# Performance work log

Hardware: AMD Instinct MI355X
Metric: run time of the kernel (lower is better)

Reference implementation:

```python
import jax, jax.numpy as jnp
import numpy as np

B, N, E, D, H = 8, 5000, 160000, 64, 128  # batch, nodes, edges, gnn hidden, head hidden


def _w(key, shape, scale=0.05):
    return jax.random.normal(key, shape, jnp.float32) * scale


def setup_inputs() -> dict:
    key = jax.random.key(0)
    ks = jax.random.split(key, 24)
    inp = {
        "x": jax.random.normal(ks[0], (B, N), jnp.float32),
        "edges": jax.random.randint(ks[1], (E, 2), 0, N, dtype=jnp.int32),
        "emb": _w(ks[2], (N, D)),
        # conv1: prepare FFN (2 layers, no bias, elu), update FFN (2 layers, bias)
        "c1_pw1": _w(ks[3], (D, D)), "c1_pw2": _w(ks[4], (D, D)),
        "c1_uw1": _w(ks[5], (2 * D, D)), "c1_ub1": jnp.zeros((D,), jnp.float32),
        "c1_uw2": _w(ks[6], (D, D)), "c1_ub2": jnp.zeros((D,), jnp.float32),
        # conv2
        "c2_pw1": _w(ks[7], (D, D)), "c2_pw2": _w(ks[8], (D, D)),
        "c2_uw1": _w(ks[9], (2 * D, D)), "c2_ub1": jnp.zeros((D,), jnp.float32),
        "c2_uw2": _w(ks[10], (D, D)), "c2_ub2": jnp.zeros((D,), jnp.float32),
        # TARnet prob heads: flatten -> Dense(H, elu) -> Dense(2) (mu, log_sigma)
        "w0a": _w(ks[11], (N * D, H), 0.005), "b0a": jnp.zeros((H,), jnp.float32),
        "w0b": _w(ks[12], (H, 2)), "b0b": jnp.zeros((2,), jnp.float32),
        "w1a": _w(ks[13], (N * D, H), 0.005), "b1a": jnp.zeros((H,), jnp.float32),
        "w1b": _w(ks[14], (H, 2)), "b1b": jnp.zeros((2,), jnp.float32),
    }
    return inp


def _graph_conv(h, edges, pw1, pw2, uw1, ub1, uw2, ub2):
    # h: [B, N, D]; edges: [E, 2] (parent, node)
    parents = jnp.take(h, edges[:, 0], axis=1)            # [B, E, D] gather
    m = jax.nn.elu(parents @ pw1)                          # prepare FFN (no bias)
    m = jax.nn.elu(m @ pw2)
    agg = jnp.zeros_like(h).at[:, edges[:, 1]].add(m)      # unsorted_segment_sum -> [B, N, D]
    hcat = jnp.concatenate([h, agg], axis=-1)              # combination_type='concat'
    u = jax.nn.elu(hcat @ uw1 + ub1)                       # update FFN
    return u @ uw2 + ub2                                   # final_activation=None


def reference(x, edges, emb,
              c1_pw1, c1_pw2, c1_uw1, c1_ub1, c1_uw2, c1_ub2,
              c2_pw1, c2_pw2, c2_uw1, c2_ub1, c2_uw2, c2_ub2,
              w0a, b0a, w0b, b0b, w1a, b1a, w1b, b1b):
    # node features scale learned per-node embeddings -> [B, N, D]
    h = x[:, :, None] * emb[None, :, :]
    h = _graph_conv(h, edges, c1_pw1, c1_pw2, c1_uw1, c1_ub1, c1_uw2, c1_ub2)
    h = _graph_conv(h, edges, c2_pw1, c2_pw2, c2_uw1, c2_ub1, c2_uw2, c2_ub2)
    phi = h.reshape(h.shape[0], -1)                        # flatten [B, N*D]
    y0 = jax.nn.elu(phi @ w0a + b0a) @ w0b + b0b           # [B, 2] (mu, log_sigma)
    y1 = jax.nn.elu(phi @ w1a + b1a) @ w1b + b1b           # [B, 2]
    return jnp.concatenate([y0, y1], axis=1)               # [B, 4]
```

## Files before the change

kernel.cpp:

```cpp
#include <hip/hip_runtime.h>


constexpr int B = 8, N = 5000, E = 160000, D = 64, H = 128;
constexpr int BN = B * N;
constexpr int ND = N * D;
constexpr long BND = (long)BN * D;

__device__ __forceinline__ float elu_f(float x) {
    return x > 0.0f ? x : __expf(x) - 1.0f;
}

__global__ __launch_bounds__(256) void k_scale(const float* __restrict__ x,
                                               const float* __restrict__ emb,
                                               float* __restrict__ h) {
    int idx = blockIdx.x * 256 + threadIdx.x;
    int d4 = idx & 15;
    int bn = idx >> 4;
    int n  = bn % N;
    float xs = x[bn];
    float4 e = reinterpret_cast<const float4*>(emb)[n * (D / 4) + d4];
    reinterpret_cast<float4*>(h)[idx] = make_float4(xs * e.x, xs * e.y, xs * e.z, xs * e.w);
}

__global__ __launch_bounds__(256) void k_count(const int* __restrict__ edges,
                                               int* __restrict__ cnt) {
    int i = blockIdx.x * 256 + threadIdx.x;
    if (i < E) atomicAdd(&cnt[edges[2 * i + 1]], 1);
}

__global__ __launch_bounds__(256) void k_scan(const int* __restrict__ cnt,
                                              int* __restrict__ offs) {
    __shared__ int part[256];
    int t = threadIdx.x;
    const int CH = 20;
    int base = t * CH;
    int s = 0;
    for (int i = 0; i < CH; ++i) { int idx = base + i; if (idx < N) s += cnt[idx]; }
    part[t] = s;
    __syncthreads();
    for (int off = 1; off < 256; off <<= 1) {
        int add = (t >= off) ? part[t - off] : 0;
        __syncthreads();
        part[t] += add;
        __syncthreads();
    }
    int run = part[t] - s;
    for (int i = 0; i < CH; ++i) {
        int idx = base + i;
        if (idx < N) { offs[idx] = run; run += cnt[idx]; }
    }
    if (t == 255) offs[N] = run;
}

__global__ __launch_bounds__(256) void k_fill(const int* __restrict__ edges,
                                              const int* __restrict__ offs,
                                              int* __restrict__ cursor,
                                              int* __restrict__ elist) {
    int i = blockIdx.x * 256 + threadIdx.x;
    if (i < E) {
        int child = edges[2 * i + 1];
        int pos = offs[child] + atomicAdd(&cursor[child], 1);
        elist[pos] = edges[2 * i];
    }
}

__global__ __launch_bounds__(256) void k_prepare(const float* __restrict__ hin,
                                                 const float* __restrict__ W1,
                                                 const float* __restrict__ W2,
                                                 float* __restrict__ M) {
    __shared__ float sW1[64 * 64];
    __shared__ float sW2[64 * 64];
    __shared__ float sP[64 * 65];
    int t = threadIdx.x;
    long r0 = (long)blockIdx.x * 64;
    for (int i = t; i < 4096; i += 256) { sW1[i] = W1[i]; sW2[i] = W2[i]; }
    int lane = t & 63, rq = t >> 6;
    for (int r = rq; r < 64; r += 4)
        sP[r * 65 + lane] = hin[(r0 + r) * 64 + lane];
    __syncthreads();

    int cg = t & 15, rg = t >> 4;
    float acc[4][4] = {};
    #pragma unroll 8
    for (int k = 0; k < 64; ++k) {
        float a[4];
        #pragma unroll
        for (int i = 0; i < 4; ++i) a[i] = sP[(rg * 4 + i) * 65 + k];
        float4 bb = *reinterpret_cast<const float4*>(&sW1[k * 64 + cg * 4]);
        #pragma unroll
        for (int i = 0; i < 4; ++i) {
            acc[i][0] += a[i] * bb.x; acc[i][1] += a[i] * bb.y;
            acc[i][2] += a[i] * bb.z; acc[i][3] += a[i] * bb.w;
        }
    }
    __syncthreads();
    #pragma unroll
    for (int i = 0; i < 4; ++i)
        #pragma unroll
        for (int j = 0; j < 4; ++j)
            sP[(rg * 4 + i) * 65 + cg * 4 + j] = elu_f(acc[i][j]);
    __syncthreads();

    float acc2[4][4] = {};
    #pragma unroll 8
    for (int k = 0; k < 64; ++k) {
        float a[4];
        #pragma unroll
        for (int i = 0; i < 4; ++i) a[i] = sP[(rg * 4 + i) * 65 + k];
        float4 bb = *reinterpret_cast<const float4*>(&sW2[k * 64 + cg * 4]);
        #pragma unroll
        for (int i = 0; i < 4; ++i) {
            acc2[i][0] += a[i] * bb.x; acc2[i][1] += a[i] * bb.y;
            acc2[i][2] += a[i] * bb.z; acc2[i][3] += a[i] * bb.w;
        }
    }
    #pragma unroll
    for (int i = 0; i < 4; ++i) {
        float4 o = make_float4(elu_f(acc2[i][0]), elu_f(acc2[i][1]),
                               elu_f(acc2[i][2]), elu_f(acc2[i][3]));
        *reinterpret_cast<float4*>(&M[(r0 + rg * 4 + i) * 64 + cg * 4]) = o;
    }
}

__global__ __launch_bounds__(256) void k_aggregate(const float* __restrict__ M,
                                                   const int* __restrict__ offs,
                                                   const int* __restrict__ elist,
                                                   float* __restrict__ agg) {
    int t = threadIdx.x;
    int lane = t & 63, unit = t >> 6;
    long bn = (long)blockIdx.x * 4 + unit;
    int b = (int)(bn / N);
    int n = (int)(bn - (long)b * N);
    int e0 = offs[n], e1 = offs[n + 1];
    const float* Mb = M + (long)b * N * 64;
    float acc = 0.0f;
    for (int e = e0; e < e1; ++e) {
        int p = elist[e];
        acc += Mb[(long)p * 64 + lane];
    }
    agg[bn * 64 + lane] = acc;
}

__global__ __launch_bounds__(256) void k_update1(const float* __restrict__ h,
                                                 const float* __restrict__ agg,
                                                 const float* __restrict__ W,
                                                 const float* __restrict__ bias,
                                                 float* __restrict__ u) {
    __shared__ float sW[128 * 64];
    __shared__ float sP[32 * 129];
    int t = threadIdx.x;
    long r0 = (long)blockIdx.x * 32;
    for (int i = t; i < 128 * 64; i += 256) sW[i] = W[i];
    for (int i = t; i < 32 * 128; i += 256) {
        int r = i >> 7, k = i & 127;
        long row = r0 + r;
        float v = (k < 64) ? h[row * 64 + k] : agg[row * 64 + (k - 64)];
        sP[r * 129 + k] = v;
    }
    __syncthreads();
    int cg = t & 15, rg = t >> 4;
    float acc[2][4] = {};
    #pragma unroll 8
    for (int k = 0; k < 128; ++k) {
        float a0 = sP[(rg * 2 + 0) * 129 + k];
        float a1 = sP[(rg * 2 + 1) * 129 + k];
        float4 bb = *reinterpret_cast<const float4*>(&sW[k * 64 + cg * 4]);
        acc[0][0] += a0 * bb.x; acc[0][1] += a0 * bb.y; acc[0][2] += a0 * bb.z; acc[0][3] += a0 * bb.w;
        acc[1][0] += a1 * bb.x; acc[1][1] += a1 * bb.y; acc[1][2] += a1 * bb.z; acc[1][3] += a1 * bb.w;
    }
    float4 b4 = *reinterpret_cast<const float4*>(&bias[cg * 4]);
    #pragma unroll
    for (int i = 0; i < 2; ++i) {
        float4 o = make_float4(elu_f(acc[i][0] + b4.x), elu_f(acc[i][1] + b4.y),
                               elu_f(acc[i][2] + b4.z), elu_f(acc[i][3] + b4.w));
        *reinterpret_cast<float4*>(&u[(r0 + rg * 2 + i) * 64 + cg * 4]) = o;
    }
}

__global__ __launch_bounds__(256) void k_update2(const float* __restrict__ u,
                                                 const float* __restrict__ W,
                                                 const float* __restrict__ bias,
                                                 float* __restrict__ hout) {
    __shared__ float sW[64 * 64];
    __shared__ float sP[32 * 65];
    int t = threadIdx.x;
    long r0 = (long)blockIdx.x * 32;
    for (int i = t; i < 4096; i += 256) sW[i] = W[i];
    for (int i = t; i < 32 * 64; i += 256) {
        int r = i >> 6, k = i & 63;
        sP[r * 65 + k] = u[(r0 + r) * 64 + k];
    }
    __syncthreads();
    int cg = t & 15, rg = t >> 4;
    float acc[2][4] = {};
    #pragma unroll 8
    for (int k = 0; k < 64; ++k) {
        float a0 = sP[(rg * 2 + 0) * 65 + k];
        float a1 = sP[(rg * 2 + 1) * 65 + k];
        float4 bb = *reinterpret_cast<const float4*>(&sW[k * 64 + cg * 4]);
        acc[0][0] += a0 * bb.x; acc[0][1] += a0 * bb.y; acc[0][2] += a0 * bb.z; acc[0][3] += a0 * bb.w;
        acc[1][0] += a1 * bb.x; acc[1][1] += a1 * bb.y; acc[1][2] += a1 * bb.z; acc[1][3] += a1 * bb.w;
    }
    float4 b4 = *reinterpret_cast<const float4*>(&bias[cg * 4]);
    #pragma unroll
    for (int i = 0; i < 2; ++i) {
        float4 o = make_float4(acc[i][0] + b4.x, acc[i][1] + b4.y,
                               acc[i][2] + b4.z, acc[i][3] + b4.w);
        *reinterpret_cast<float4*>(&hout[(r0 + rg * 2 + i) * 64 + cg * 4]) = o;
    }
}

__global__ __launch_bounds__(128) void k_head(const float* __restrict__ phi,
                                              const float* __restrict__ w0a,
                                              const float* __restrict__ w1a,
                                              float* __restrict__ hidden) {
    const float* wa = blockIdx.y ? w1a : w0a;
    float* hid = hidden + blockIdx.y * (8 * H);
    int h = threadIdx.x;
    int k0 = blockIdx.x * 320;
    float acc[8] = {};
    #pragma unroll 8
    for (int kk = 0; kk < 320; ++kk) {
        int k = k0 + kk;
        float w = wa[(long)k * H + h];
        #pragma unroll
        for (int b2 = 0; b2 < 8; ++b2)
            acc[b2] += phi[b2 * ND + k] * w;
    }
    #pragma unroll
    for (int b2 = 0; b2 < 8; ++b2)
        unsafeAtomicAdd(&hid[b2 * H + h], acc[b2]);
}

__global__ __launch_bounds__(64) void k_final(const float* __restrict__ hidden,
                                              const float* __restrict__ b0a,
                                              const float* __restrict__ w0b,
                                              const float* __restrict__ b0b,
                                              const float* __restrict__ b1a,
                                              const float* __restrict__ w1b,
                                              const float* __restrict__ b1b,
                                              float* __restrict__ out) {
    int t = threadIdx.x;
    if (t >= 32) return;
    int head = t >> 4, b = (t >> 1) & 7, j = t & 1;
    const float* hid = hidden + head * (8 * H) + b * H;
    const float* ba = head ? b1a : b0a;
    const float* wb = head ? w1b : w0b;
    const float* bb = head ? b1b : b0b;
    float acc = 0.0f;
    for (int hh = 0; hh < H; ++hh)
        acc += elu_f(hid[hh] + ba[hh]) * wb[hh * 2 + j];
    out[b * 4 + head * 2 + j] = acc + bb[j];
}

extern "C" void kernel_launch(void* const* d_in, const int* in_sizes, int n_in,
                              void* d_out, int out_size, void* d_ws, size_t ws_size,
                              hipStream_t stream) {
    const float* x      = (const float*)d_in[0];
    const int*   edges  = (const int*)d_in[1];
    const float* emb    = (const float*)d_in[2];
    const float* c1_pw1 = (const float*)d_in[3];
    const float* c1_pw2 = (const float*)d_in[4];
    const float* c1_uw1 = (const float*)d_in[5];
    const float* c1_ub1 = (const float*)d_in[6];
    const float* c1_uw2 = (const float*)d_in[7];
    const float* c1_ub2 = (const float*)d_in[8];
    const float* c2_pw1 = (const float*)d_in[9];
    const float* c2_pw2 = (const float*)d_in[10];
    const float* c2_uw1 = (const float*)d_in[11];
    const float* c2_ub1 = (const float*)d_in[12];
    const float* c2_uw2 = (const float*)d_in[13];
    const float* c2_ub2 = (const float*)d_in[14];
    const float* w0a    = (const float*)d_in[15];
    const float* b0a    = (const float*)d_in[16];
    const float* w0b    = (const float*)d_in[17];
    const float* b0b    = (const float*)d_in[18];
    const float* w1a    = (const float*)d_in[19];
    const float* b1a    = (const float*)d_in[20];
    const float* w1b    = (const float*)d_in[21];
    const float* b1b    = (const float*)d_in[22];
    float* out = (float*)d_out;

    float* hA     = (float*)d_ws;
    float* hB     = hA + BND;
    float* Mu     = hB + BND;
    float* agg    = Mu + BND;
    float* hidden = agg + BND;
    int* cnt      = (int*)(hidden + 2048);
    int* offs     = cnt + N;
    int* cursor   = offs + N + 1;
    int* elist    = cursor + N;

    hipMemsetAsync(cnt, 0, N * sizeof(int), stream);
    hipMemsetAsync(cursor, 0, N * sizeof(int), stream);
    hipMemsetAsync(hidden, 0, 2 * 8 * H * sizeof(float), stream);

    k_scale<<<2500, 256, 0, stream>>>(x, emb, hA);

    k_count<<<E / 256, 256, 0, stream>>>(edges, cnt);
    k_scan<<<1, 256, 0, stream>>>(cnt, offs);
    k_fill<<<E / 256, 256, 0, stream>>>(edges, offs, cursor, elist);

    k_prepare<<<BN / 64, 256, 0, stream>>>(hA, c1_pw1, c1_pw2, Mu);
    k_aggregate<<<BN / 4, 256, 0, stream>>>(Mu, offs, elist, agg);
    k_update1<<<BN / 32, 256, 0, stream>>>(hA, agg, c1_uw1, c1_ub1, Mu);
    k_update2<<<BN / 32, 256, 0, stream>>>(Mu, c1_uw2, c1_ub2, hB);

    k_prepare<<<BN / 64, 256, 0, stream>>>(hB, c2_pw1, c2_pw2, Mu);
    k_aggregate<<<BN / 4, 256, 0, stream>>>(Mu, offs, elist, agg);
    k_update1<<<BN / 32, 256, 0, stream>>>(hB, agg, c2_uw1, c2_ub1, Mu);
    k_update2<<<BN / 32, 256, 0, stream>>>(Mu, c2_uw2, c2_ub2, hA);

    k_head<<<dim3(ND / 320, 2), 128, 0, stream>>>(hA, w0a, w1a, hidden);
    k_final<<<1, 64, 0, stream>>>(hidden, b0a, w0b, b0b, b1a, w1b, b1b, out);
}
```

Before: 730.4 us.

## Fuse scale into prepare, merge update kernels, vectorize aggregate and head GEMV

```diff
diff --git a/kernel.cpp b/kernel.cpp
--- a/kernel.cpp
+++ b/kernel.cpp
@@ -5,21 +5,10 @@
 constexpr int BN = B * N;
 constexpr int ND = N * D;
 constexpr long BND = (long)BN * D;
+constexpr int KC = 640;
 
 __device__ __forceinline__ float elu_f(float x) {
     return x > 0.0f ? x : __expf(x) - 1.0f;
-}
-
-__global__ __launch_bounds__(256) void k_scale(const float* __restrict__ x,
-                                               const float* __restrict__ emb,
-                                               float* __restrict__ h) {
-    int idx = blockIdx.x * 256 + threadIdx.x;
-    int d4 = idx & 15;
-    int bn = idx >> 4;
-    int n  = bn % N;
-    float xs = x[bn];
-    float4 e = reinterpret_cast<const float4*>(emb)[n * (D / 4) + d4];
-    reinterpret_cast<float4*>(h)[idx] = make_float4(xs * e.x, xs * e.y, xs * e.z, xs * e.w);
 }
 
 __global__ __launch_bounds__(256) void k_count(const int* __restrict__ edges,
@@ -64,24 +53,42 @@
     }
 }
 
-__global__ __launch_bounds__(256) void k_prepare(const float* __restrict__ hin,
+__global__ __launch_bounds__(512) void k_prepare(const float* __restrict__ xsrc,
+                                                 const float* __restrict__ emb,
+                                                 const float* __restrict__ hin,
                                                  const float* __restrict__ W1,
                                                  const float* __restrict__ W2,
-                                                 float* __restrict__ M) {
+                                                 float* __restrict__ M,
+                                                 float* __restrict__ hwt) {
     __shared__ float sW1[64 * 64];
-    __shared__ float sW2[64 * 64];
-    __shared__ float sP[64 * 65];
-    int t = threadIdx.x;
-    long r0 = (long)blockIdx.x * 64;
-    for (int i = t; i < 4096; i += 256) { sW1[i] = W1[i]; sW2[i] = W2[i]; }
-    int lane = t & 63, rq = t >> 6;
-    for (int r = rq; r < 64; r += 4)
-        sP[r * 65 + lane] = hin[(r0 + r) * 64 + lane];
+    __shared__ float sP[128 * 65];
+    int t = threadIdx.x;
+    int r0 = blockIdx.x * 128;
+    for (int i = t; i < 4096; i += 512) sW1[i] = W1[i];
+    if (xsrc) {
+        for (int i = t; i < 128 * 64; i += 512) {
+            int r = i >> 6, c = i & 63;
+            int row = r0 + r;
+            float v = 0.0f;
+            if (row < BN) {
+                int n = row % N;
+                v = xsrc[row] * emb[n * 64 + c];
+                hwt[(long)row * 64 + c] = v;
+            }
+            sP[r * 65 + c] = v;
+        }
+    } else {
+        for (int i = t; i < 128 * 64; i += 512) {
+            int r = i >> 6, c = i & 63;
+            int row = r0 + r;
+            sP[r * 65 + c] = (row < BN) ? hin[(long)row * 64 + c] : 0.0f;
+        }
+    }
     __syncthreads();
 
     int cg = t & 15, rg = t >> 4;
     float acc[4][4] = {};
-    #pragma unroll 8
+    #pragma unroll 4
     for (int k = 0; k < 64; ++k) {
         float a[4];
         #pragma unroll
@@ -102,12 +109,12 @@
     __syncthreads();
 
     float acc2[4][4] = {};
-    #pragma unroll 8
+    #pragma unroll 4
     for (int k = 0; k < 64; ++k) {
         float a[4];
         #pragma unroll
         for (int i = 0; i < 4; ++i) a[i] = sP[(rg * 4 + i) * 65 + k];
-        float4 bb = *reinterpret_cast<const float4*>(&sW2[k * 64 + cg * 4]);
+        float4 bb = *reinterpret_cast<const float4*>(&W2[k * 64 + cg * 4]);
         #pragma unroll
         for (int i = 0; i < 4; ++i) {
             acc2[i][0] += a[i] * bb.x; acc2[i][1] += a[i] * bb.y;
@@ -116,9 +123,12 @@
     }
     #pragma unroll
     for (int i = 0; i < 4; ++i) {
-        float4 o = make_float4(elu_f(acc2[i][0]), elu_f(acc2[i][1]),
-                               elu_f(acc2[i][2]), elu_f(acc2[i][3]));
-        *reinterpret_cast<float4*>(&M[(r0 + rg * 4 + i) * 64 + cg * 4]) = o;
+        int row = r0 + rg * 4 + i;
+        if (row < BN) {
+            float4 o = make_float4(elu_f(acc2[i][0]), elu_f(acc2[i][1]),
+                                   elu_f(acc2[i][2]), elu_f(acc2[i][3]));
+            *reinterpret_cast<float4*>(&M[(long)row * 64 + cg * 4]) = o;
+        }
     }
 }
 
@@ -127,109 +137,146 @@
                                                    const int* __restrict__ elist,
                                                    float* __restrict__ agg) {
     int t = threadIdx.x;
-    int lane = t & 63, unit = t >> 6;
-    long bn = (long)blockIdx.x * 4 + unit;
-    int b = (int)(bn / N);
-    int n = (int)(bn - (long)b * N);
+    int lane = t & 63, wv = t >> 6;
+    int bn = blockIdx.x * 4 + wv;
+    int b = bn / N;
+    int n = bn - b * N;
     int e0 = offs[n], e1 = offs[n + 1];
-    const float* Mb = M + (long)b * N * 64;
-    float acc = 0.0f;
-    for (int e = e0; e < e1; ++e) {
+    const float* Mb = M + (long)b * ND;
+    int h4 = lane & 15, le = lane >> 4;
+    float4 acc = make_float4(0.f, 0.f, 0.f, 0.f);
+    for (int e = e0 + le; e < e1; e += 4) {
         int p = elist[e];
-        acc += Mb[(long)p * 64 + lane];
-    }
-    agg[bn * 64 + lane] = acc;
-}
-
-__global__ __launch_bounds__(256) void k_update1(const float* __restrict__ h,
-                                                 const float* __restrict__ agg,
-                                                 const float* __restrict__ W,
-                                                 const float* __restrict__ bias,
-                                                 float* __restrict__ u) {
-    __shared__ float sW[128 * 64];
-    __shared__ float sP[32 * 129];
-    int t = threadIdx.x;
-    long r0 = (long)blockIdx.x * 32;
-    for (int i = t; i < 128 * 64; i += 256) sW[i] = W[i];
-    for (int i = t; i < 32 * 128; i += 256) {
+        float4 v = *reinterpret_cast<const float4*>(&Mb[(long)p * 64 + h4 * 4]);
+        acc.x += v.x; acc.y += v.y; acc.z += v.z; acc.w += v.w;
+    }
+    #pragma unroll
+    for (int m = 16; m <= 32; m <<= 1) {
+        acc.x += __shfl_xor(acc.x, m);
+        acc.y += __shfl_xor(acc.y, m);
+        acc.z += __shfl_xor(acc.z, m);
+        acc.w += __shfl_xor(acc.w, m);
+    }
+    if (le == 0)
+        *reinterpret_cast<float4*>(&agg[(long)bn * 64 + h4 * 4]) = acc;
+}
+
+__global__ __launch_bounds__(512) void k_update(const float* __restrict__ h,
+                                                const float* __restrict__ agg,
+                                                const float* __restrict__ W1,
+                                                const float* __restrict__ b1,
+                                                const float* __restrict__ W2,
+                                                const float* __restrict__ b2,
+                                                float* __restrict__ hout) {
+    __shared__ float sW1[128 * 64];
+    __shared__ float sP[64 * 129];
+    int t = threadIdx.x;
+    long r0 = (long)blockIdx.x * 64;
+    for (int i = t; i < 128 * 64; i += 512) sW1[i] = W1[i];
+    for (int i = t; i < 64 * 128; i += 512) {
         int r = i >> 7, k = i & 127;
         long row = r0 + r;
         float v = (k < 64) ? h[row * 64 + k] : agg[row * 64 + (k - 64)];
         sP[r * 129 + k] = v;
     }
     __syncthreads();
+
     int cg = t & 15, rg = t >> 4;
     float acc[2][4] = {};
-    #pragma unroll 8
+    #pragma unroll 4
     for (int k = 0; k < 128; ++k) {
         float a0 = sP[(rg * 2 + 0) * 129 + k];
         float a1 = sP[(rg * 2 + 1) * 129 + k];
-        float4 bb = *reinterpret_cast<const float4*>(&sW[k * 64 + cg * 4]);
+        float4 bb = *reinterpret_cast<const float4*>(&sW1[k * 64 + cg * 4]);
         acc[0][0] += a0 * bb.x; acc[0][1] += a0 * bb.y; acc[0][2] += a0 * bb.z; acc[0][3] += a0 * bb.w;
         acc[1][0] += a1 * bb.x; acc[1][1] += a1 * bb.y; acc[1][2] += a1 * bb.z; acc[1][3] += a1 * bb.w;
     }
-    float4 b4 = *reinterpret_cast<const float4*>(&bias[cg * 4]);
+    float4 bv1 = *reinterpret_cast<const float4*>(&b1[cg * 4]);
+    __syncthreads();
     #pragma unroll
     for (int i = 0; i < 2; ++i) {
-        float4 o = make_float4(elu_f(acc[i][0] + b4.x), elu_f(acc[i][1] + b4.y),
-                               elu_f(acc[i][2] + b4.z), elu_f(acc[i][3] + b4.w));
-        *reinterpret_cast<float4*>(&u[(r0 + rg * 2 + i) * 64 + cg * 4]) = o;
-    }
-}
-
-__global__ __launch_bounds__(256) void k_update2(const float* __restrict__ u,
-                                                 const float* __restrict__ W,
-                                                 const float* __restrict__ bias,
-                                                 float* __restrict__ hout) {
-    __shared__ float sW[64 * 64];
-    __shared__ float sP[32 * 65];
-    int t = threadIdx.x;
-    long r0 = (long)blockIdx.x * 32;
-    for (int i = t; i < 4096; i += 256) sW[i] = W[i];
-    for (int i = t; i < 32 * 64; i += 256) {
-        int r = i >> 6, k = i & 63;
-        sP[r * 65 + k] = u[(r0 + r) * 64 + k];
-    }
-    __syncthreads();
-    int cg = t & 15, rg = t >> 4;
-    float acc[2][4] = {};
-    #pragma unroll 8
+        sP[(rg * 2 + i) * 129 + cg * 4 + 0] = elu_f(acc[i][0] + bv1.x);
+        sP[(rg * 2 + i) * 129 + cg * 4 + 1] = elu_f(acc[i][1] + bv1.y);
+        sP[(rg * 2 + i) * 129 + cg * 4 + 2] = elu_f(acc[i][2] + bv1.z);
+        sP[(rg * 2 + i) * 129 + cg * 4 + 3] = elu_f(acc[i][3] + bv1.w);
+    }
+    __syncthreads();
+
+    float acc2[2][4] = {};
+    #pragma unroll 4
     for (int k = 0; k < 64; ++k) {
-        float a0 = sP[(rg * 2 + 0) * 65 + k];
-        float a1 = sP[(rg * 2 + 1) * 65 + k];
-        float4 bb = *reinterpret_cast<const float4*>(&sW[k * 64 + cg * 4]);
-        acc[0][0] += a0 * bb.x; acc[0][1] += a0 * bb.y; acc[0][2] += a0 * bb.z; acc[0][3] += a0 * bb.w;
-        acc[1][0] += a1 * bb.x; acc[1][1] += a1 * bb.y; acc[1][2] += a1 * bb.z; acc[1][3] += a1 * bb.w;
-    }
-    float4 b4 = *reinterpret_cast<const float4*>(&bias[cg * 4]);
+        float a0 = sP[(rg * 2 + 0) * 129 + k];
+        float a1 = sP[(rg * 2 + 1) * 129 + k];
+        float4 bb = *reinterpret_cast<const float4*>(&W2[k * 64 + cg * 4]);
+        acc2[0][0] += a0 * bb.x; acc2[0][1] += a0 * bb.y; acc2[0][2] += a0 * bb.z; acc2[0][3] += a0 * bb.w;
+        acc2[1][0] += a1 * bb.x; acc2[1][1] += a1 * bb.y; acc2[1][2] += a1 * bb.z; acc2[1][3] += a1 * bb.w;
+    }
+    float4 bv2 = *reinterpret_cast<const float4*>(&b2[cg * 4]);
     #pragma unroll
     for (int i = 0; i < 2; ++i) {
-        float4 o = make_float4(acc[i][0] + b4.x, acc[i][1] + b4.y,
-                               acc[i][2] + b4.z, acc[i][3] + b4.w);
+        float4 o = make_float4(acc2[i][0] + bv2.x, acc2[i][1] + bv2.y,
+                               acc2[i][2] + bv2.z, acc2[i][3] + bv2.w);
         *reinterpret_cast<float4*>(&hout[(r0 + rg * 2 + i) * 64 + cg * 4]) = o;
     }
 }
 
-__global__ __launch_bounds__(128) void k_head(const float* __restrict__ phi,
+__global__ __launch_bounds__(256) void k_head(const float* __restrict__ phi,
                                               const float* __restrict__ w0a,
                                               const float* __restrict__ w1a,
                                               float* __restrict__ hidden) {
+    __shared__ float smem[8 * 32 * 33];
     const float* wa = blockIdx.y ? w1a : w0a;
     float* hid = hidden + blockIdx.y * (8 * H);
-    int h = threadIdx.x;
-    int k0 = blockIdx.x * 320;
-    float acc[8] = {};
-    #pragma unroll 8
-    for (int kk = 0; kk < 320; ++kk) {
-        int k = k0 + kk;
-        float w = wa[(long)k * H + h];
-        #pragma unroll
-        for (int b2 = 0; b2 < 8; ++b2)
-            acc[b2] += phi[b2 * ND + k] * w;
-    }
-    #pragma unroll
-    for (int b2 = 0; b2 < 8; ++b2)
-        unsafeAtomicAdd(&hid[b2 * H + h], acc[b2]);
+    int t = threadIdx.x;
+    int k0 = blockIdx.x * KC;
+
+    #pragma unroll
+    for (int b = 0; b < 8; ++b)
+        for (int kk = t; kk < KC; kk += 256)
+            smem[b * KC + kk] = phi[(long)b * ND + k0 + kk];
+    __syncthreads();
+
+    int h4 = t & 31, kl = t >> 5;
+    const float* wp = wa + (long)(k0 + kl) * H + h4 * 4;
+    float4 acc[8];
+    #pragma unroll
+    for (int b = 0; b < 8; ++b) acc[b] = make_float4(0.f, 0.f, 0.f, 0.f);
+
+    #pragma unroll 4
+    for (int it = 0; it < KC / 8; ++it) {
+        float4 w4 = *reinterpret_cast<const float4*>(wp + (long)it * 8 * H);
+        int kk = it * 8 + kl;
+        #pragma unroll
+        for (int b = 0; b < 8; ++b) {
+            float p = smem[b * KC + kk];
+            acc[b].x += p * w4.x; acc[b].y += p * w4.y;
+            acc[b].z += p * w4.z; acc[b].w += p * w4.w;
+        }
+    }
+    __syncthreads();
+
+    int base = (kl * 32 + h4) * 33;
+    #pragma unroll
+    for (int b = 0; b < 8; ++b) {
+        smem[base + b * 4 + 0] = acc[b].x;
+        smem[base + b * 4 + 1] = acc[b].y;
+        smem[base + b * 4 + 2] = acc[b].z;
+        smem[base + b * 4 + 3] = acc[b].w;
+    }
+    __syncthreads();
+
+    int rh4 = t & 31, rb = t >> 5;
+    float s0 = 0.f, s1 = 0.f, s2 = 0.f, s3 = 0.f;
+    #pragma unroll
+    for (int klr = 0; klr < 8; ++klr) {
+        int idx = (klr * 32 + rh4) * 33 + rb * 4;
+        s0 += smem[idx + 0]; s1 += smem[idx + 1];
+        s2 += smem[idx + 2]; s3 += smem[idx + 3];
+    }
+    unsafeAtomicAdd(&hid[rb * H + rh4 * 4 + 0], s0);
+    unsafeAtomicAdd(&hid[rb * H + rh4 * 4 + 1], s1);
+    unsafeAtomicAdd(&hid[rb * H + rh4 * 4 + 2], s2);
+    unsafeAtomicAdd(&hid[rb * H + rh4 * 4 + 3], s3);
 }
 
 __global__ __launch_bounds__(64) void k_final(const float* __restrict__ hidden,
@@ -287,30 +334,24 @@
     float* agg    = Mu + BND;
     float* hidden = agg + BND;
     int* cnt      = (int*)(hidden + 2048);
-    int* offs     = cnt + N;
-    int* cursor   = offs + N + 1;
-    int* elist    = cursor + N;
-
-    hipMemsetAsync(cnt, 0, N * sizeof(int), stream);
-    hipMemsetAsync(cursor, 0, N * sizeof(int), stream);
-    hipMemsetAsync(hidden, 0, 2 * 8 * H * sizeof(float), stream);
-
-    k_scale<<<2500, 256, 0, stream>>>(x, emb, hA);
-
-    k_count<<<E / 256, 256, 0, stream>>>(edges, cnt);
+    int* cursor   = cnt + N;
+    int* offs     = cursor + N;
+    int* elist    = offs + N + 1;
+
+    hipMemsetAsync(hidden, 0, (2048 + 2 * N) * sizeof(float), stream);
+
+    k_count<<<(E + 255) / 256, 256, 0, stream>>>(edges, cnt);
     k_scan<<<1, 256, 0, stream>>>(cnt, offs);
-    k_fill<<<E / 256, 256, 0, stream>>>(edges, offs, cursor, elist);
-
-    k_prepare<<<BN / 64, 256, 0, stream>>>(hA, c1_pw1, c1_pw2, Mu);
+    k_fill<<<(E + 255) / 256, 256, 0, stream>>>(edges, offs, cursor, elist);
+
+    k_prepare<<<(BN + 127) / 128, 512, 0, stream>>>(x, emb, nullptr, c1_pw1, c1_pw2, Mu, hA);
     k_aggregate<<<BN / 4, 256, 0, stream>>>(Mu, offs, elist, agg);
-    k_update1<<<BN / 32, 256, 0, stream>>>(hA, agg, c1_uw1, c1_ub1, Mu);
-    k_update2<<<BN / 32, 256, 0, stream>>>(Mu, c1_uw2, c1_ub2, hB);
-
-    k_prepare<<<BN / 64, 256, 0, stream>>>(hB, c2_pw1, c2_pw2, Mu);
+    k_update<<<BN / 64, 512, 0, stream>>>(hA, agg, c1_uw1, c1_ub1, c1_uw2, c1_ub2, hB);
+
+    k_prepare<<<(BN + 127) / 128, 512, 0, stream>>>(nullptr, emb, hB, c2_pw1, c2_pw2, Mu, nullptr);
     k_aggregate<<<BN / 4, 256, 0, stream>>>(Mu, offs, elist, agg);
-    k_update1<<<BN / 32, 256, 0, stream>>>(hB, agg, c2_uw1, c2_ub1, Mu);
-    k_update2<<<BN / 32, 256, 0, stream>>>(Mu, c2_uw2, c2_ub2, hA);
-
-    k_head<<<dim3(ND / 320, 2), 128, 0, stream>>>(hA, w0a, w1a, hidden);
+    k_update<<<BN / 64, 512, 0, stream>>>(hB, agg, c2_uw1, c2_ub1, c2_uw2, c2_ub2, hA);
+
+    k_head<<<dim3(ND / KC, 2), 256, 0, stream>>>(hA, w0a, w1a, hidden);
     k_final<<<1, 64, 0, stream>>>(hidden, b0a, w0b, b0b, b1a, w1b, b1b, out);
 }
```

After: 651.5 us. -10.8%, faster.
